# Kernel tuning notes

Hardware: AMD Instinct MI355X
Metric: run time of the kernel (lower is better)

The kernel has to match this reference:

```python
import jax, jax.numpy as jnp
import numpy as np

N = 100_000      # nodes
E = 1_600_000    # edges (avg degree 16)
F_IN = 128       # dataset.num_features
H = 128          # hidden
C = 25_000       # num_clusters (~ target_ratio 0.25 * N)
G = 64           # graphs in batch
NCLS = 10        # dataset.num_classes


def _gcn_conv(x, w, b, src, dst, n):
    # PyG GCNConv: add self loops, symmetric normalization deg^-1/2 A_hat deg^-1/2
    h = x @ w  # [n, out]
    deg = jnp.zeros((n,), x.dtype).at[dst].add(1.0) + 1.0  # +1 self loop
    dis = jax.lax.rsqrt(deg)
    norm = dis[src] * dis[dst]  # [E]
    out = jnp.zeros_like(h).at[dst].add(h[src] * norm[:, None])
    out = out + h * (dis * dis)[:, None]  # self-loop term norm_ii = deg_i^-1
    return out + b


def _mean_pool(x, seg, num_seg):
    s = jax.ops.segment_sum(x, seg, num_segments=num_seg)
    cnt = jax.ops.segment_sum(jnp.ones((x.shape[0],), x.dtype), seg, num_segments=num_seg)
    return s / jnp.maximum(cnt, 1.0)[:, None]


def _max_pool(x, seg, num_seg):
    m = jax.ops.segment_max(x, seg, num_segments=num_seg)
    cnt = jax.ops.segment_sum(jnp.ones((x.shape[0],), x.dtype), seg, num_segments=num_seg)
    return jnp.where(cnt[:, None] > 0, m, 0.0)


def setup_inputs() -> dict:
    key = jax.random.key(0)
    ks = jax.random.split(key, 12)
    def glorot(k, shape):
        fan_in = shape[0]
        return (jax.random.normal(k, shape, jnp.float32) / np.sqrt(fan_in)).astype(jnp.float32)
    return {
        "x": jax.random.normal(ks[0], (N, F_IN), jnp.float32),
        "edge_index": jax.random.randint(ks[1], (2, E), 0, N, dtype=jnp.int32).astype(jnp.int64),
        "batch": jnp.sort(jax.random.randint(ks[2], (N,), 0, G, dtype=jnp.int32)).astype(jnp.int64),
        "cluster": jax.random.randint(ks[3], (N,), 0, C, dtype=jnp.int32).astype(jnp.int64),
        "num_clusters": C,
        "num_graphs": G,
        "W1": glorot(ks[4], (F_IN, H)), "b1": jnp.zeros((H,), jnp.float32),
        "W2": glorot(ks[5], (H, H)),   "b2": jnp.zeros((H,), jnp.float32),
        "W3": glorot(ks[6], (H, H)),   "b3": jnp.zeros((H,), jnp.float32),
        "lin1_w": glorot(ks[7], (4 * H, H)), "lin1_b": jnp.zeros((H,), jnp.float32),
        "lin2_w": glorot(ks[8], (H, NCLS)),  "lin2_b": jnp.zeros((NCLS,), jnp.float32),
    }


def reference(x, edge_index, batch, cluster, num_clusters, num_graphs,
              W1, b1, W2, b2, W3, b3, lin1_w, lin1_b, lin2_w, lin2_b):
    n = x.shape[0]
    src, dst = edge_index[0], edge_index[1]
    # conv1 + relu (dropout is identity in eval mode)
    h = jax.nn.relu(_gcn_conv(x, W1, b1, src, dst, n))
    pre_mean = _mean_pool(h, batch, num_graphs)
    pre_max = _max_pool(h, batch, num_graphs)
    # LaCorePooling(aggregate='mean'): segment-mean nodes by cluster id,
    # relabel edges to cluster ids, derive pooled batch vector.
    hp = _mean_pool(h, cluster, num_clusters)            # [C, H]
    src_p, dst_p = cluster[src], cluster[dst]            # pooled edge list
    batch_p = jax.ops.segment_max(batch, cluster, num_segments=num_clusters)
    batch_p = jnp.maximum(batch_p, 0)                    # empty clusters -> graph 0
    # post-pool GCN layers
    hp = jax.nn.relu(_gcn_conv(hp, W2, b2, src_p, dst_p, num_clusters))
    hp = jax.nn.relu(_gcn_conv(hp, W3, b3, src_p, dst_p, num_clusters))
    post_mean = _mean_pool(hp, batch_p, num_graphs)
    post_max = _max_pool(hp, batch_p, num_graphs)
    z = jnp.concatenate([pre_mean, pre_max, post_mean, post_max], axis=-1)  # [G, 4H]
    z = jax.nn.relu(z @ lin1_w + lin1_b)
    z = z @ lin2_w + lin2_b
    return jax.nn.log_softmax(z, axis=-1)
```

## Files before the change

### kernel.cpp

```cpp
#include <hip/hip_runtime.h>

constexpr int N_NODES = 100000;
constexpr int N_EDGES = 1600000;
constexpr int N_CLUST = 25000;
constexpr int N_GRAPH = 64;
constexpr int NCLSN   = 10;

constexpr int BKT1_SHIFT = 9;
constexpr int NBKT1 = (N_NODES + 511) / 512;
constexpr int EPB = 4096;
constexpr int NEB = (N_EDGES + EPB - 1) / EPB;
constexpr int SORT_CAP = 12288;

constexpr int SCAN_BPB = 1024;
constexpr int NB1 = (N_NODES + SCAN_BPB - 1) / SCAN_BPB;
constexpr int NB2 = (N_CLUST + SCAN_BPB - 1) / SCAN_BPB;
constexpr int NB3 = (N_CLUST + SCAN_BPB - 1) / SCAN_BPB;
constexpr int NBT = NB1 + NB2 + NB3;

__device__ __forceinline__ float bf16lo(unsigned u){ return __uint_as_float(u << 16); }
__device__ __forceinline__ float bf16hi(unsigned u){ return __uint_as_float(u & 0xffff0000u); }
__device__ __forceinline__ unsigned bf16_rne(float f){
  unsigned u = __float_as_uint(f);
  return (u + 0x7fffu + ((u >> 16) & 1u)) >> 16;
}
__device__ __forceinline__ unsigned pack2(float lo, float hi){
  return bf16_rne(lo) | (bf16_rne(hi) << 16);
}

typedef short bf16x8 __attribute__((ext_vector_type(8)));
typedef float f32x4  __attribute__((ext_vector_type(4)));

__launch_bounds__(1024)
__global__ void count_kernel(const int* __restrict__ ei, int* __restrict__ bhist){
  __shared__ int h1c[NBKT1];
  int t = threadIdx.x;
  for (int i = t; i < NBKT1; i += 1024) h1c[i] = 0;
  __syncthreads();
  int e0 = blockIdx.x * EPB;
  #pragma unroll
  for (int i = 0; i < EPB / 1024; ++i){
    int e = e0 + i * 1024 + t;
    if (e < N_EDGES) atomicAdd(&h1c[ei[N_EDGES + e] >> BKT1_SHIFT], 1);
  }
  __syncthreads();
  for (int i = t; i < NBKT1; i += 1024) bhist[blockIdx.x * NBKT1 + i] = h1c[i];
}

__launch_bounds__(512)
__global__ void colscan(const int* __restrict__ bhist, int* __restrict__ boffs,
                        int* __restrict__ gcnt1){
  __shared__ int s[512];
  int i = blockIdx.x;
  int t = threadIdx.x;
  int v = (t < NEB) ? bhist[t * NBKT1 + i] : 0;
  s[t] = v; __syncthreads();
  for (int o = 1; o < 512; o <<= 1){
    int a = (t >= o) ? s[t - o] : 0;
    __syncthreads(); s[t] += a; __syncthreads();
  }
  if (t < NEB) boffs[t * NBKT1 + i] = s[t] - v;
  if (t == 511) gcnt1[i] = s[511];
}

__launch_bounds__(256)
__global__ void bucket_scan(const int* __restrict__ gcnt1, int* __restrict__ gbase1){
  __shared__ int s[256];
  int t = threadIdx.x;
  int v = (t < NBKT1) ? gcnt1[t] : 0;
  s[t] = v; __syncthreads();
  for (int off = 1; off < 256; off <<= 1){
    int a = (t >= off) ? s[t - off] : 0;
    __syncthreads(); s[t] += a; __syncthreads();
  }
  if (t < NBKT1) gbase1[t] = s[t] - v;
}

__launch_bounds__(1024)
__global__ void scatter_kernel(const int* __restrict__ ei, const int* __restrict__ gbase1,
                               const int* __restrict__ boffs, unsigned int* __restrict__ stage1){
  __shared__ int gb1[NBKT1];
  __shared__ int cur[NBKT1];
  int t = threadIdx.x, b = blockIdx.x;
  for (int i = t; i < NBKT1; i += 1024){
    gb1[i] = gbase1[i] + boffs[b * NBKT1 + i];
    cur[i] = 0;
  }
  __syncthreads();
  int e0 = b * EPB;
  #pragma unroll
  for (int i = 0; i < EPB / 1024; ++i){
    int e = e0 + i * 1024 + t;
    if (e < N_EDGES){
      int src = ei[e], dst = ei[N_EDGES + e];
      int bk = dst >> BKT1_SHIFT;
      int r = atomicAdd(&cur[bk], 1);
      stage1[gb1[bk] + r] = ((unsigned)(dst & 511) << 17) | (unsigned)src;
    }
  }
}

__launch_bounds__(1024)
__global__ void bucket_sort(const unsigned int* __restrict__ stage, const int* __restrict__ gbase,
                            const int* __restrict__ gcnt, int* __restrict__ outpay,
                            int* __restrict__ deg){
  __shared__ int cnt[512], off[512];
  __shared__ int sorted[SORT_CAP];
  int b = blockIdx.x, t = threadIdx.x;
  int base = gbase[b], n = gcnt[b];
  if (t < 512) cnt[t] = 0;
  __syncthreads();
  for (int i = t; i < n; i += 1024) atomicAdd(&cnt[stage[base + i] >> 17], 1);
  __syncthreads();
  if (t < 512){
    int idx = b * 512 + t;
    if (idx < N_NODES) deg[idx] = cnt[t];
    off[t] = cnt[t];
  }
  __syncthreads();
  for (int s = 1; s < 512; s <<= 1){
    int v = 0;
    if (t < 512 && t >= s) v = off[t - s];
    __syncthreads();
    if (t < 512) off[t] += v;
    __syncthreads();
  }
  if (t < 512) off[t] -= cnt[t];
  __syncthreads();
  if (n <= SORT_CAP){
    for (int i = t; i < n; i += 1024){
      unsigned w = stage[base + i];
      int r = atomicAdd(&off[w >> 17], 1);
      sorted[r] = (int)(w & 0x1FFFFu);
    }
    __syncthreads();
    for (int i = t; i < n; i += 1024) outpay[base + i] = sorted[i];
  } else {
    for (int i = t; i < n; i += 1024){
      unsigned w = stage[base + i];
      int r = atomicAdd(&off[w >> 17], 1);
      outpay[base + r] = (int)(w & 0x1FFFFu);
    }
  }
}

__global__ void node_prep(const int* __restrict__ cluster, const int* __restrict__ deg1,
                          int* __restrict__ cntn, int* __restrict__ deg2){
  int v = blockIdx.x * blockDim.x + threadIdx.x;
  if (v < N_NODES){
    int c = cluster[v];
    atomicAdd(&cntn[c], 1);
    atomicAdd(&deg2[c], deg1[v]);
  }
}

__device__ __forceinline__ void seg_select(int b, const int* deg1, const int* cntn,
                                           const int* deg2, const int*& src, int& n, int& base){
  if (b < NB1){ src = deg1; n = N_NODES; base = b * SCAN_BPB; }
  else if (b < NB1 + NB2){ src = cntn; n = N_CLUST; base = (b - NB1) * SCAN_BPB; }
  else { src = deg2; n = N_CLUST; base = (b - NB1 - NB2) * SCAN_BPB; }
}

__launch_bounds__(256)
__global__ void block_sums(const int* __restrict__ deg1, const int* __restrict__ cntn,
                           const int* __restrict__ deg2, int* __restrict__ bsum){
  int b = blockIdx.x;
  const int* src; int n, base;
  seg_select(b, deg1, cntn, deg2, src, n, base);
  int t = threadIdx.x;
  int i0 = base + t * 4;
  int s = 0;
  if (i0 + 3 < n){ int4 v = *(const int4*)&src[i0]; s = v.x + v.y + v.z + v.w; }
  else { for (int j = 0; j < 4; ++j){ int i = i0 + j; if (i < n) s += src[i]; } }
  __shared__ int sh[256];
  sh[t] = s; __syncthreads();
  for (int off = 128; off > 0; off >>= 1){
    if (t < off) sh[t] += sh[t + off];
    __syncthreads();
  }
  if (t == 0) bsum[b] = sh[0];
}

__launch_bounds__(256)
__global__ void scan_bsums(const int* __restrict__ bsum, int* __restrict__ boff,
                           int* __restrict__ rowptr1, int* __restrict__ rowptrn,
                           int* __restrict__ rowptr2){
  __shared__ int s[256];
  int t = threadIdx.x;
  int v = (t < NBT) ? bsum[t] : 0;
  s[t] = v; __syncthreads();
  int seg = (t < NB1) ? 0 : (t < NB1 + NB2 ? 1 : 2);
  for (int off = 1; off < 256; off <<= 1){
    int add = 0;
    if (t >= off){
      int u = t - off;
      int useg = (u < NB1) ? 0 : (u < NB1 + NB2 ? 1 : 2);
      if (useg == seg) add = s[u];
    }
    __syncthreads();
    s[t] += add;
    __syncthreads();
  }
  if (t < NBT) boff[t] = s[t] - v;
  if (t == NB1 - 1)       rowptr1[N_NODES] = s[t];
  if (t == NB1 + NB2 - 1) rowptrn[N_CLUST] = s[t];
  if (t == NBT - 1)       rowptr2[N_CLUST] = s[t];
}

__launch_bounds__(256)
__global__ void scan_final(const int* __restrict__ deg1, const int* __restrict__ cntn,
                           const int* __restrict__ deg2, const int* __restrict__ boff,
                           int* __restrict__ rowptr1, float* __restrict__ dis1,
                           int* __restrict__ rowptrn, int* __restrict__ curn,
                           int* __restrict__ rowptr2, float* __restrict__ dis2){
  int b = blockIdx.x;
  const int* src; int n, base;
  seg_select(b, deg1, cntn, deg2, src, n, base);
  int* rp; int* cur; float* dis;
  if (b < NB1){ rp = rowptr1; cur = nullptr; dis = dis1; }
  else if (b < NB1 + NB2){ rp = rowptrn; cur = curn; dis = nullptr; }
  else { rp = rowptr2; cur = nullptr; dis = dis2; }
  int t = threadIdx.x;
  int i0 = base + t * 4;
  int v[4]; int s = 0;
  #pragma unroll
  for (int j = 0; j < 4; ++j){ int i = i0 + j; v[j] = (i < n) ? src[i] : 0; s += v[j]; }
  __shared__ int sh[256];
  sh[t] = s; __syncthreads();
  for (int off = 1; off < 256; off <<= 1){
    int add = (t >= off) ? sh[t - off] : 0;
    __syncthreads();
    sh[t] += add;
    __syncthreads();
  }
  int run = sh[t] - s + boff[b];
  #pragma unroll
  for (int j = 0; j < 4; ++j){
    int i = i0 + j;
    if (i < n){
      rp[i] = run;
      if (cur) cur[i] = run;
      if (dis) dis[i] = rsqrtf((float)v[j] + 1.0f);
      run += v[j];
    }
  }
}

__global__ void fill_n(const int* __restrict__ cluster, int* __restrict__ curn,
                       int* __restrict__ nidx){
  int v = blockIdx.x * blockDim.x + threadIdx.x;
  if (v >= N_NODES) return;
  nidx[atomicAdd(&curn[cluster[v]], 1)] = v;
}

__launch_bounds__(256)
__global__ void psrc_build(const int* __restrict__ rowptrn, const int* __restrict__ nidx,
                           const int* __restrict__ rowptr1, const int* __restrict__ esrc1,
                           const int* __restrict__ cluster, const int* __restrict__ rowptr2,
                           int* __restrict__ psrcC){
  int c = blockIdx.x * 4 + (threadIdx.x >> 6);
  int l = threadIdx.x & 63;
  int mb = rowptrn[c], me = rowptrn[c + 1];
  int cnt = me - mb;
  int base_l = 0, d_l = 0;
  if (l < cnt){
    int v = nidx[mb + l];
    base_l = rowptr1[v];
    d_l = rowptr1[v + 1] - base_l;
  }
  int pref = d_l;
  #pragma unroll
  for (int off = 1; off < 64; off <<= 1){
    int u = __shfl_up(pref, off);
    if (l >= off) pref += u;
  }
  int total = __shfl(pref, 63);
  int wbase = rowptr2[c];
  int iters = (total + 63) >> 6;
  for (int k = 0; k < iters; ++k){
    int idx = k * 64 + l;
    int idxc = min(idx, total - 1);
    int m = 0;
    for (int j = 0; j < cnt; ++j){
      int pj = __shfl(pref, j);
      if (idxc >= pj) m = j + 1;
    }
    int pm = __shfl(pref, m);
    int dm = __shfl(d_l, m);
    int bm = __shfl(base_l, m);
    int e = bm + idxc - (pm - dm);
    int sc = cluster[esrc1[e]];
    if (idx < total) psrcC[wbase + idx] = sc;
  }
}

template<bool A_BF16>
__launch_bounds__(256)
__global__ void gemm_mfma(const void* __restrict__ Aptr, const float* __restrict__ B,
                          const float* __restrict__ scale, unsigned* __restrict__ Cmat,
                          int M){
  __shared__ __align__(16) unsigned Blds[128 * 68];
  __shared__ __align__(16) unsigned Alds[64 * 68];
  const int t = threadIdx.x;
  const int row0 = blockIdx.x * 64;

  #pragma unroll
  for (int i = 0; i < 8; ++i){
    int task = t + i * 256;
    int kp = task >> 5, nq = task & 31;
    float4 b0 = *(const float4*)&B[(2 * kp) * 128 + nq * 4];
    float4 b1 = *(const float4*)&B[(2 * kp + 1) * 128 + nq * 4];
    Blds[(nq * 4 + 0) * 68 + kp] = pack2(b0.x, b1.x);
    Blds[(nq * 4 + 1) * 68 + kp] = pack2(b0.y, b1.y);
    Blds[(nq * 4 + 2) * 68 + kp] = pack2(b0.z, b1.z);
    Blds[(nq * 4 + 3) * 68 + kp] = pack2(b0.w, b1.w);
  }
  if (A_BF16){
    const unsigned* A = (const unsigned*)Aptr;
    #pragma unroll
    for (int i = 0; i < 8; ++i){
      int idx = t + i * 256;
      int row = idx >> 5, c2 = idx & 31;
      int grow = min(row0 + row, M - 1);
      uint2 v = *(const uint2*)&A[(size_t)grow * 64 + c2 * 2];
      Alds[row * 68 + c2 * 2]     = v.x;
      Alds[row * 68 + c2 * 2 + 1] = v.y;
    }
  } else {
    const float* A = (const float*)Aptr;
    #pragma unroll
    for (int i = 0; i < 8; ++i){
      int idx = t + i * 256;
      int row = idx >> 5, k4 = idx & 31;
      int grow = min(row0 + row, M - 1);
      float4 v = *(const float4*)&A[(size_t)grow * 128 + k4 * 4];
      Alds[row * 68 + k4 * 2]     = pack2(v.x, v.y);
      Alds[row * 68 + k4 * 2 + 1] = pack2(v.z, v.w);
    }
  }
  __syncthreads();

  const int wv = t >> 6, l = t & 63, quad = l >> 4, n16 = l & 15;
  f32x4 acc[8];
  #pragma unroll
  for (int nt = 0; nt < 8; ++nt) acc[nt] = (f32x4){0.f, 0.f, 0.f, 0.f};
  const int arow = wv * 16 + n16;
  #pragma unroll
  for (int ks = 0; ks < 4; ++ks){
    bf16x8 af = *(const bf16x8*)&Alds[arow * 68 + ks * 16 + quad * 4];
    #pragma unroll
    for (int nt = 0; nt < 8; ++nt){
      bf16x8 bfr = *(const bf16x8*)&Blds[(nt * 16 + n16) * 68 + ks * 16 + quad * 4];
      acc[nt] = __builtin_amdgcn_mfma_f32_16x16x32_bf16(af, bfr, acc[nt], 0, 0, 0);
    }
  }
  #pragma unroll
  for (int nt = 0; nt < 8; ++nt){
    #pragma unroll
    for (int r = 0; r < 4; ++r){
      int row = row0 + wv * 16 + quad * 4 + r;
      float sc = scale[min(row, M - 1)];
      float v = acc[nt][r] * sc;
      float vhi = __shfl_xor(v, 1);
      if (((l & 1) == 0) && row < M)
        Cmat[(size_t)row * 64 + nt * 8 + (n16 >> 1)] = pack2(v, vhi);
    }
  }
}

__launch_bounds__(256)
__global__ void conv_csr(const unsigned* __restrict__ Ts, const float* __restrict__ dis,
                         const int* __restrict__ rowptr, const int* __restrict__ esrc,
                         const float* __restrict__ bias, unsigned* __restrict__ Hout){
  int w = blockIdx.x * 4 + (threadIdx.x >> 6);
  int l = threadIdx.x & 63;
  int q = l & 15, h = l >> 4;
  int beg = rowptr[w], end = rowptr[w + 1];
  float acc[8] = {0.f,0.f,0.f,0.f,0.f,0.f,0.f,0.f};
  for (int base = beg; base < end; base += 64){
    int n = min(64, end - base);
    int eid = esrc[base + min(l, n - 1)];
    int j = 0;
    for (; j + 8 <= n; j += 8){
      int s0 = __shfl(eid, j + h);
      int s1 = __shfl(eid, j + 4 + h);
      uint4 u0 = *(const uint4*)&Ts[(size_t)s0 * 64 + q * 4];
      uint4 u1 = *(const uint4*)&Ts[(size_t)s1 * 64 + q * 4];
      acc[0] += bf16lo(u0.x); acc[1] += bf16hi(u0.x);
      acc[2] += bf16lo(u0.y); acc[3] += bf16hi(u0.y);
      acc[4] += bf16lo(u0.z); acc[5] += bf16hi(u0.z);
      acc[6] += bf16lo(u0.w); acc[7] += bf16hi(u0.w);
      acc[0] += bf16lo(u1.x); acc[1] += bf16hi(u1.x);
      acc[2] += bf16lo(u1.y); acc[3] += bf16hi(u1.y);
      acc[4] += bf16lo(u1.z); acc[5] += bf16hi(u1.z);
      acc[6] += bf16lo(u1.w); acc[7] += bf16hi(u1.w);
    }
    for (; j < n; j += 4){
      int ei = j + h;
      int s = __shfl(eid, min(ei, n - 1));
      uint4 u = *(const uint4*)&Ts[(size_t)s * 64 + q * 4];
      if (ei < n){
        acc[0] += bf16lo(u.x); acc[1] += bf16hi(u.x);
        acc[2] += bf16lo(u.y); acc[3] += bf16hi(u.y);
        acc[4] += bf16lo(u.z); acc[5] += bf16hi(u.z);
        acc[6] += bf16lo(u.w); acc[7] += bf16hi(u.w);
      }
    }
  }
  #pragma unroll
  for (int k = 0; k < 8; ++k){
    acc[k] += __shfl_xor(acc[k], 16);
    acc[k] += __shfl_xor(acc[k], 32);
  }
  float d = dis[w];
  uint4 us = *(const uint4*)&Ts[(size_t)w * 64 + q * 4];
  float4 b0 = *(const float4*)&bias[q * 8];
  float4 b1 = *(const float4*)&bias[q * 8 + 4];
  float r0 = fmaxf(fmaf(d, acc[0] + bf16lo(us.x), b0.x), 0.f);
  float r1 = fmaxf(fmaf(d, acc[1] + bf16hi(us.x), b0.y), 0.f);
  float r2 = fmaxf(fmaf(d, acc[2] + bf16lo(us.y), b0.z), 0.f);
  float r3 = fmaxf(fmaf(d, acc[3] + bf16hi(us.y), b0.w), 0.f);
  float r4 = fmaxf(fmaf(d, acc[4] + bf16lo(us.z), b1.x), 0.f);
  float r5 = fmaxf(fmaf(d, acc[5] + bf16hi(us.z), b1.y), 0.f);
  float r6 = fmaxf(fmaf(d, acc[6] + bf16lo(us.w), b1.z), 0.f);
  float r7 = fmaxf(fmaf(d, acc[7] + bf16hi(us.w), b1.w), 0.f);
  if (h == 0){
    uint4 o;
    o.x = pack2(r0, r1); o.y = pack2(r2, r3);
    o.z = pack2(r4, r5); o.w = pack2(r6, r7);
    *(uint4*)&Hout[(size_t)w * 64 + q * 4] = o;
  }
}

__launch_bounds__(256)
__global__ void cluster_gather(const unsigned* __restrict__ h1, const int* __restrict__ rowptrn,
                               const int* __restrict__ nidx, const int* __restrict__ batch,
                               unsigned* __restrict__ hp, int* __restrict__ batchp){
  int c = blockIdx.x * 4 + (threadIdx.x >> 6);
  int l = threadIdx.x & 63;
  int q = l & 15, h = l >> 4;
  int mb = rowptrn[c], me = rowptrn[c + 1];
  float acc[8] = {0.f,0.f,0.f,0.f,0.f,0.f,0.f,0.f};
  int vmax = -1;
  for (int base = mb; base < me; base += 64){
    int n = min(64, me - base);
    int vid = nidx[base + min(l, n - 1)];
    if (l < n) vmax = max(vmax, vid);
    int j = 0;
    for (; j + 8 <= n; j += 8){
      int s0 = __shfl(vid, j + h);
      int s1 = __shfl(vid, j + 4 + h);
      uint4 u0 = *(const uint4*)&h1[(size_t)s0 * 64 + q * 4];
      uint4 u1 = *(const uint4*)&h1[(size_t)s1 * 64 + q * 4];
      acc[0] += bf16lo(u0.x); acc[1] += bf16hi(u0.x);
      acc[2] += bf16lo(u0.y); acc[3] += bf16hi(u0.y);
      acc[4] += bf16lo(u0.z); acc[5] += bf16hi(u0.z);
      acc[6] += bf16lo(u0.w); acc[7] += bf16hi(u0.w);
      acc[0] += bf16lo(u1.x); acc[1] += bf16hi(u1.x);
      acc[2] += bf16lo(u1.y); acc[3] += bf16hi(u1.y);
      acc[4] += bf16lo(u1.z); acc[5] += bf16hi(u1.z);
      acc[6] += bf16lo(u1.w); acc[7] += bf16hi(u1.w);
    }
    for (; j < n; j += 4){
      int ei = j + h;
      int s = __shfl(vid, min(ei, n - 1));
      uint4 u = *(const uint4*)&h1[(size_t)s * 64 + q * 4];
      if (ei < n){
        acc[0] += bf16lo(u.x); acc[1] += bf16hi(u.x);
        acc[2] += bf16lo(u.y); acc[3] += bf16hi(u.y);
        acc[4] += bf16lo(u.z); acc[5] += bf16hi(u.z);
        acc[6] += bf16lo(u.w); acc[7] += bf16hi(u.w);
      }
    }
  }
  #pragma unroll
  for (int k = 0; k < 8; ++k){
    acc[k] += __shfl_xor(acc[k], 16);
    acc[k] += __shfl_xor(acc[k], 32);
  }
  #pragma unroll
  for (int off = 32; off > 0; off >>= 1) vmax = max(vmax, __shfl_xor(vmax, off));
  float inv = 1.0f / (float)max(me - mb, 1);
  if (h == 0){
    uint4 o;
    o.x = pack2(acc[0] * inv, acc[1] * inv);
    o.y = pack2(acc[2] * inv, acc[3] * inv);
    o.z = pack2(acc[4] * inv, acc[5] * inv);
    o.w = pack2(acc[6] * inv, acc[7] * inv);
    *(uint4*)&hp[(size_t)c * 64 + q * 4] = o;
  }
  if (l == 0) batchp[c] = (vmax >= 0) ? batch[vmax] : 0;
}

__global__ void cntp_kernel(const int* __restrict__ batchp, int* __restrict__ cntp){
  int c = blockIdx.x * blockDim.x + threadIdx.x;
  if (c < N_CLUST) atomicAdd(&cntp[batchp[c]], 1);
}

__global__ void scan_cntp(const int* __restrict__ cntp, int* __restrict__ gbasep,
                          int* __restrict__ curp){
  int t = threadIdx.x;
  int v = cntp[t];
  int s = v;
  for (int off = 1; off < 64; off <<= 1){
    int u = __shfl_up(s, off);
    if (t >= off) s += u;
  }
  gbasep[t] = s - v; curp[t] = s - v;
  if (t == 63) gbasep[64] = s;
}

__global__ void fill_c(const int* __restrict__ batchp, int* __restrict__ curp,
                       int* __restrict__ cidx){
  int c = blockIdx.x * blockDim.x + threadIdx.x;
  if (c < N_CLUST) cidx[atomicAdd(&curp[batchp[c]], 1)] = c;
}

__global__ void graph_bounds(const int* __restrict__ batch, int* __restrict__ gstart){
  int g = threadIdx.x;
  if (g > N_GRAPH) return;
  int lo = 0, hi = N_NODES;
  while (lo < hi){ int mid = (lo + hi) >> 1; if (batch[mid] < g) lo = mid + 1; else hi = mid; }
  gstart[g] = lo;
}

__device__ __forceinline__ void atomicMaxPosF(float* addr, float v){
  atomicMax((int*)addr, __float_as_int(v));
}

constexpr int PRE_SPLIT = 8;
__launch_bounds__(256)
__global__ void pre_pool_g(const unsigned* __restrict__ h1, const int* __restrict__ gstart,
                           float* __restrict__ psum, float* __restrict__ pmax){
  int g = blockIdx.x / PRE_SPLIT, sp = blockIdx.x % PRE_SPLIT;
  int t = threadIdx.x, w = t >> 6, l = t & 63;
  int s0 = gstart[g], s1 = gstart[g + 1];
  int n = s1 - s0;
  int per = (n + PRE_SPLIT - 1) / PRE_SPLIT;
  int b0 = s0 + sp * per, b1 = min(b0 + per, s1);
  float2 a0{0.f,0.f}, a1{0.f,0.f}, a2{0.f,0.f}, a3{0.f,0.f};
  float2 mx{0.f,0.f};
  int i = b0 + w;
  for (; i + 12 < b1; i += 16){
    unsigned u0 = h1[(size_t)(i     ) * 64 + l];
    unsigned u1 = h1[(size_t)(i +  4) * 64 + l];
    unsigned u2 = h1[(size_t)(i +  8) * 64 + l];
    unsigned u3 = h1[(size_t)(i + 12) * 64 + l];
    float f0x = bf16lo(u0), f0y = bf16hi(u0);
    float f1x = bf16lo(u1), f1y = bf16hi(u1);
    float f2x = bf16lo(u2), f2y = bf16hi(u2);
    float f3x = bf16lo(u3), f3y = bf16hi(u3);
    a0.x += f0x; a0.y += f0y; a1.x += f1x; a1.y += f1y;
    a2.x += f2x; a2.y += f2y; a3.x += f3x; a3.y += f3y;
    mx.x = fmaxf(fmaxf(mx.x, fmaxf(f0x, f1x)), fmaxf(f2x, f3x));
    mx.y = fmaxf(fmaxf(mx.y, fmaxf(f0y, f1y)), fmaxf(f2y, f3y));
  }
  for (; i < b1; i += 4){
    unsigned u = h1[(size_t)i * 64 + l];
    float fx = bf16lo(u), fy = bf16hi(u);
    a0.x += fx; a0.y += fy;
    mx.x = fmaxf(mx.x, fx); mx.y = fmaxf(mx.y, fy);
  }
  __shared__ float2 ssum[4][64], smax[4][64];
  ssum[w][l] = { a0.x + a1.x + a2.x + a3.x, a0.y + a1.y + a2.y + a3.y };
  smax[w][l] = mx;
  __syncthreads();
  if (w == 0){
    float2 S = ssum[0][l], M = smax[0][l];
    #pragma unroll
    for (int k = 1; k < 4; ++k){
      S.x += ssum[k][l].x; S.y += ssum[k][l].y;
      M.x = fmaxf(M.x, smax[k][l].x); M.y = fmaxf(M.y, smax[k][l].y);
    }
    atomicAdd(&psum[g * 128 + 2 * l], S.x);
    atomicAdd(&psum[g * 128 + 2 * l + 1], S.y);
    atomicMaxPosF(&pmax[g * 128 + 2 * l], M.x);
    atomicMaxPosF(&pmax[g * 128 + 2 * l + 1], M.y);
  }
}

constexpr int POST_SPLIT = 4;
__launch_bounds__(256)
__global__ void post_pool_g(const unsigned* __restrict__ hp3, const int* __restrict__ gbasep,
                            const int* __restrict__ cidx,
                            float* __restrict__ psum, float* __restrict__ pmax){
  int g = blockIdx.x / POST_SPLIT, sp = blockIdx.x % POST_SPLIT;
  int t = threadIdx.x, w = t >> 6, l = t & 63;
  int s0 = gbasep[g], s1 = gbasep[g + 1];
  int n = s1 - s0;
  int per = (n + POST_SPLIT * 4 - 1) / (POST_SPLIT * 4);
  int b0 = s0 + (sp * 4 + w) * per, b1 = min(b0 + per, s1);
  float2 a0{0.f,0.f}, a1{0.f,0.f}, a2{0.f,0.f}, a3{0.f,0.f};
  float2 mx{0.f,0.f};
  for (int base = b0; base < b1; base += 64){
    int nn = min(64, b1 - base);
    int cid = cidx[base + min(l, nn - 1)];
    int j = 0;
    for (; j + 4 <= nn; j += 4){
      int c0 = __shfl(cid, j);
      int c1 = __shfl(cid, j + 1);
      int c2 = __shfl(cid, j + 2);
      int c3 = __shfl(cid, j + 3);
      unsigned u0 = hp3[(size_t)c0 * 64 + l];
      unsigned u1 = hp3[(size_t)c1 * 64 + l];
      unsigned u2 = hp3[(size_t)c2 * 64 + l];
      unsigned u3 = hp3[(size_t)c3 * 64 + l];
      float f0x = bf16lo(u0), f0y = bf16hi(u0);
      float f1x = bf16lo(u1), f1y = bf16hi(u1);
      float f2x = bf16lo(u2), f2y = bf16hi(u2);
      float f3x = bf16lo(u3), f3y = bf16hi(u3);
      a0.x += f0x; a0.y += f0y; a1.x += f1x; a1.y += f1y;
      a2.x += f2x; a2.y += f2y; a3.x += f3x; a3.y += f3y;
      mx.x = fmaxf(fmaxf(mx.x, fmaxf(f0x, f1x)), fmaxf(f2x, f3x));
      mx.y = fmaxf(fmaxf(mx.y, fmaxf(f0y, f1y)), fmaxf(f2y, f3y));
    }
    for (; j < nn; ++j){
      int c = __shfl(cid, j);
      unsigned u = hp3[(size_t)c * 64 + l];
      float fx = bf16lo(u), fy = bf16hi(u);
      a0.x += fx; a0.y += fy;
      mx.x = fmaxf(mx.x, fx); mx.y = fmaxf(mx.y, fy);
    }
  }
  __shared__ float2 ssum[4][64], smax[4][64];
  ssum[w][l] = { a0.x + a1.x + a2.x + a3.x, a0.y + a1.y + a2.y + a3.y };
  smax[w][l] = mx;
  __syncthreads();
  if (w == 0){
    float2 S = ssum[0][l], M = smax[0][l];
    #pragma unroll
    for (int k = 1; k < 4; ++k){
      S.x += ssum[k][l].x; S.y += ssum[k][l].y;
      M.x = fmaxf(M.x, smax[k][l].x); M.y = fmaxf(M.y, smax[k][l].y);
    }
    atomicAdd(&psum[g * 128 + 2 * l], S.x);
    atomicAdd(&psum[g * 128 + 2 * l + 1], S.y);
    atomicMaxPosF(&pmax[g * 128 + 2 * l], M.x);
    atomicMaxPosF(&pmax[g * 128 + 2 * l + 1], M.y);
  }
}

__launch_bounds__(128)
__global__ void head_kernel(const float* __restrict__ psum, const float* __restrict__ pmax,
                            const float* __restrict__ postsum, const float* __restrict__ postmax,
                            const int* __restrict__ gstart, const int* __restrict__ cntp,
                            const float* __restrict__ l1w, const float* __restrict__ l1b,
                            const float* __restrict__ l2w, const float* __restrict__ l2b,
                            float* __restrict__ out){
  int g = blockIdx.x, t = threadIdx.x;
  __shared__ float z[512];
  __shared__ float a[128];
  __shared__ float logits[16];
  __shared__ float lse_s;
  float cpre  = (float)max(gstart[g + 1] - gstart[g], 1);
  float cpost = fmaxf((float)cntp[g], 1.0f);
  z[t]       = psum[g * 128 + t] / cpre;
  z[128 + t] = pmax[g * 128 + t];
  z[256 + t] = postsum[g * 128 + t] / cpost;
  z[384 + t] = postmax[g * 128 + t];
  __syncthreads();
  float acc = l1b[t];
  #pragma unroll 8
  for (int k = 0; k < 512; ++k) acc = fmaf(z[k], l1w[k * 128 + t], acc);
  a[t] = fmaxf(acc, 0.f);
  __syncthreads();
  if (t < NCLSN){
    float s2 = l2b[t];
    for (int k = 0; k < 128; ++k) s2 = fmaf(a[k], l2w[k * NCLSN + t], s2);
    logits[t] = s2;
  }
  __syncthreads();
  if (t == 0){
    float m = logits[0];
    for (int c = 1; c < NCLSN; ++c) m = fmaxf(m, logits[c]);
    float s = 0.f;
    for (int c = 0; c < NCLSN; ++c) s += expf(logits[c] - m);
    lse_s = m + logf(s);
  }
  __syncthreads();
  if (t < NCLSN) out[g * NCLSN + t] = logits[t] - lse_s;
}

extern "C" void kernel_launch(void* const* d_in, const int* in_sizes, int n_in,
                              void* d_out, int out_size, void* d_ws, size_t ws_size,
                              hipStream_t stream){
  const float* x       = (const float*)d_in[0];
  const int*   ei      = (const int*)  d_in[1];
  const int*   batch   = (const int*)  d_in[2];
  const int*   cluster = (const int*)  d_in[3];
  const float* W1      = (const float*)d_in[6];
  const float* b1      = (const float*)d_in[7];
  const float* W2      = (const float*)d_in[8];
  const float* b2      = (const float*)d_in[9];
  const float* W3      = (const float*)d_in[10];
  const float* b3      = (const float*)d_in[11];
  const float* l1w     = (const float*)d_in[12];
  const float* l1b     = (const float*)d_in[13];
  const float* l2w     = (const float*)d_in[14];
  const float* l2b     = (const float*)d_in[15];
  float* out = (float*)d_out;

  char* base = (char*)d_ws;
  size_t off = 0;
  auto alloc = [&](size_t bytes) -> char* {
    char* p = base + off;
    off += (bytes + 255) & ~size_t(255);
    return p;
  };
  char*  zbase  = base + off;
  int*   cntn   = (int*)  alloc((size_t)N_CLUST * 4);
  int*   deg2   = (int*)  alloc((size_t)N_CLUST * 4);
  int*   cntp   = (int*)  alloc((size_t)N_GRAPH * 4);
  float* pre_s  = (float*)alloc((size_t)N_GRAPH * 128 * 4);
  float* pre_m  = (float*)alloc((size_t)N_GRAPH * 128 * 4);
  float* post_s = (float*)alloc((size_t)N_GRAPH * 128 * 4);
  float* post_m = (float*)alloc((size_t)N_GRAPH * 128 * 4);
  size_t zsize = off;
  unsigned* Ts1   = (unsigned*)alloc((size_t)N_NODES * 64 * 4);
  unsigned* h1    = (unsigned*)alloc((size_t)N_NODES * 64 * 4);
  int*   esrc1   = (int*)  alloc((size_t)N_EDGES * 4);
  int*   psrcC   = (int*)  alloc((size_t)N_EDGES * 4);
  int*   deg1    = (int*)  alloc((size_t)N_NODES * 4);
  int*   rowptr1 = (int*)  alloc((size_t)(N_NODES + 1) * 4);
  int*   rowptrn = (int*)  alloc((size_t)(N_CLUST + 1) * 4);
  int*   curn    = (int*)  alloc((size_t)N_CLUST * 4);
  int*   rowptr2 = (int*)  alloc((size_t)(N_CLUST + 1) * 4);
  int*   nidx    = (int*)  alloc((size_t)N_NODES * 4);
  float* dis1    = (float*)alloc((size_t)N_NODES * 4);
  float* dis2    = (float*)alloc((size_t)N_CLUST * 4);
  int*   batchp  = (int*)  alloc((size_t)N_CLUST * 4);
  int*   gstart  = (int*)  alloc((size_t)(N_GRAPH + 1) * 4);
  int*   bsum    = (int*)  alloc((size_t)NBT * 4);
  int*   boff    = (int*)  alloc((size_t)NBT * 4);
  int*   gcnt1   = (int*)  alloc((size_t)NBKT1 * 4);
  int*   gbase1  = (int*)  alloc((size_t)NBKT1 * 4);
  int*   bhist   = (int*)  alloc((size_t)NEB * NBKT1 * 4);
  int*   boffs   = (int*)  alloc((size_t)NEB * NBKT1 * 4);
  int*   gbasep  = (int*)  alloc((size_t)(N_GRAPH + 1) * 4);
  int*   curp    = (int*)  alloc((size_t)N_GRAPH * 4);
  int*   cidx    = (int*)  alloc((size_t)N_CLUST * 4);
  unsigned int* stage1 = (unsigned int*)h1;
  unsigned* hp  = Ts1;
  unsigned* Ts2 = Ts1 + (size_t)N_CLUST * 64;
  unsigned* hp2 = Ts1 + (size_t)2 * N_CLUST * 64;
  unsigned* hp3 = Ts1 + (size_t)3 * N_CLUST * 64;
  unsigned* Ts3 = Ts2;

  (void)in_sizes; (void)n_in; (void)out_size; (void)ws_size;

  hipMemsetAsync(zbase, 0, zsize, stream);

  count_kernel  <<<NEB, 1024, 0, stream>>>(ei, bhist);
  colscan       <<<NBKT1, 512, 0, stream>>>(bhist, boffs, gcnt1);
  bucket_scan   <<<1, 256, 0, stream>>>(gcnt1, gbase1);
  scatter_kernel<<<NEB, 1024, 0, stream>>>(ei, gbase1, boffs, stage1);
  bucket_sort   <<<NBKT1, 1024, 0, stream>>>(stage1, gbase1, gcnt1, esrc1, deg1);
  node_prep<<<(N_NODES + 255) / 256, 256, 0, stream>>>(cluster, deg1, cntn, deg2);
  block_sums <<<NBT, 256, 0, stream>>>(deg1, cntn, deg2, bsum);
  scan_bsums <<<1, 256, 0, stream>>>(bsum, boff, rowptr1, rowptrn, rowptr2);
  scan_final <<<NBT, 256, 0, stream>>>(deg1, cntn, deg2, boff,
                                       rowptr1, dis1, rowptrn, curn, rowptr2, dis2);
  fill_n<<<(N_NODES + 255) / 256, 256, 0, stream>>>(cluster, curn, nidx);
  psrc_build<<<N_CLUST / 4, 256, 0, stream>>>(rowptrn, nidx, rowptr1, esrc1,
                                              cluster, rowptr2, psrcC);

  gemm_mfma<false><<<(N_NODES + 63) / 64, 256, 0, stream>>>(x, W1, dis1, Ts1, N_NODES);
  conv_csr<<<N_NODES / 4, 256, 0, stream>>>(Ts1, dis1, rowptr1, esrc1, b1, h1);

  graph_bounds<<<1, 128, 0, stream>>>(batch, gstart);
  pre_pool_g<<<N_GRAPH * PRE_SPLIT, 256, 0, stream>>>(h1, gstart, pre_s, pre_m);

  cluster_gather<<<N_CLUST / 4, 256, 0, stream>>>(h1, rowptrn, nidx, batch, hp, batchp);
  cntp_kernel<<<(N_CLUST + 255) / 256, 256, 0, stream>>>(batchp, cntp);
  scan_cntp<<<1, 64, 0, stream>>>(cntp, gbasep, curp);
  fill_c<<<(N_CLUST + 255) / 256, 256, 0, stream>>>(batchp, curp, cidx);

  gemm_mfma<true><<<(N_CLUST + 63) / 64, 256, 0, stream>>>(hp, W2, dis2, Ts2, N_CLUST);
  conv_csr<<<N_CLUST / 4, 256, 0, stream>>>(Ts2, dis2, rowptr2, psrcC, b2, hp2);

  gemm_mfma<true><<<(N_CLUST + 63) / 64, 256, 0, stream>>>(hp2, W3, dis2, Ts3, N_CLUST);
  conv_csr<<<N_CLUST / 4, 256, 0, stream>>>(Ts3, dis2, rowptr2, psrcC, b3, hp3);

  post_pool_g<<<N_GRAPH * POST_SPLIT, 256, 0, stream>>>(hp3, gbasep, cidx, post_s, post_m);
  head_kernel<<<N_GRAPH, 128, 0, stream>>>(pre_s, pre_m, post_s, post_m, gstart, cntp,
                                           l1w, l1b, l2w, l2b, out);
}
```

Measured before the change: 527.6 us.

## Merge small pipeline kernels into fewer launches via block-range fusion

Cuts the launch chain from about 23 kernels to 13. The memset is folded into extra blocks of the count kernel, and the bucket scan is recomputed redundantly in each scatter and sort block. Node-prep atomics move into bucket_sort, and the block-offset scan moves into scan_final. Independent work (gemm1 with fill_n, conv1 with psrc_build, cluster gather with pre-pool, gemm2 with the cluster CSR build) now shares one grid split by block index. This targets per-launch overhead and serialization gaps, at the cost of redundant scans per block and the single-block cidx fill sitting inside the gemm2 launch.

After: 606.9 us. 15.0% more time.

```diff
diff --git a/kernel.cpp b/kernel.cpp
--- a/kernel.cpp
+++ b/kernel.cpp
@@ -11,6 +11,7 @@
 constexpr int EPB = 4096;
 constexpr int NEB = (N_EDGES + EPB - 1) / EPB;
 constexpr int SORT_CAP = 12288;
+constexpr int NZB = 16;
 
 constexpr int SCAN_BPB = 1024;
 constexpr int NB1 = (N_NODES + SCAN_BPB - 1) / SCAN_BPB;
@@ -18,6 +19,16 @@
 constexpr int NB3 = (N_CLUST + SCAN_BPB - 1) / SCAN_BPB;
 constexpr int NBT = NB1 + NB2 + NB3;
 
+constexpr int G1  = (N_NODES + 63) / 64;
+constexpr int FN  = (N_NODES + 255) / 256;
+constexpr int C1  = N_NODES / 4;
+constexpr int PS  = N_CLUST / 4;
+constexpr int CG  = N_CLUST / 4;
+constexpr int PRE_SPLIT = 8;
+constexpr int PP  = N_GRAPH * PRE_SPLIT;
+constexpr int G2  = (N_CLUST + 63) / 64;
+constexpr int POST_SPLIT = 4;
+
 __device__ __forceinline__ float bf16lo(unsigned u){ return __uint_as_float(u << 16); }
 __device__ __forceinline__ float bf16hi(unsigned u){ return __uint_as_float(u & 0xffff0000u); }
 __device__ __forceinline__ unsigned bf16_rne(float f){
@@ -31,10 +42,23 @@
 typedef short bf16x8 __attribute__((ext_vector_type(8)));
 typedef float f32x4  __attribute__((ext_vector_type(4)));
 
+__device__ __forceinline__ int bsearch_batch(const int* __restrict__ batch, int g){
+  int lo = 0, hi = N_NODES;
+  while (lo < hi){ int mid = (lo + hi) >> 1; if (batch[mid] < g) lo = mid + 1; else hi = mid; }
+  return lo;
+}
+
 __launch_bounds__(1024)
-__global__ void count_kernel(const int* __restrict__ ei, int* __restrict__ bhist){
+__global__ void count_kernel(const int* __restrict__ ei, int* __restrict__ bhist,
+                             uint4* __restrict__ zbase, int zwords4){
+  int t = threadIdx.x;
+  if (blockIdx.x >= NEB){
+    int zb = blockIdx.x - NEB;
+    for (int i = zb * 1024 + t; i < zwords4; i += NZB * 1024)
+      zbase[i] = (uint4){0u, 0u, 0u, 0u};
+    return;
+  }
   __shared__ int h1c[NBKT1];
-  int t = threadIdx.x;
   for (int i = t; i < NBKT1; i += 1024) h1c[i] = 0;
   __syncthreads();
   int e0 = blockIdx.x * EPB;
@@ -63,28 +87,29 @@
   if (t == 511) gcnt1[i] = s[511];
 }
 
-__launch_bounds__(256)
-__global__ void bucket_scan(const int* __restrict__ gcnt1, int* __restrict__ gbase1){
+__device__ __forceinline__ void scan_gcnt(const int* __restrict__ gcnt1, int* s, int t){
+  if (t < 256) s[t] = (t < NBKT1) ? gcnt1[t] : 0;
+  __syncthreads();
+  for (int o = 1; o < 256; o <<= 1){
+    int a = 0;
+    if (t < 256 && t >= o) a = s[t - o];
+    __syncthreads();
+    if (t < 256) s[t] += a;
+    __syncthreads();
+  }
+}
+
+__launch_bounds__(1024)
+__global__ void scatter_kernel(const int* __restrict__ ei, const int* __restrict__ gcnt1,
+                               const int* __restrict__ boffs, unsigned int* __restrict__ stage1){
   __shared__ int s[256];
-  int t = threadIdx.x;
-  int v = (t < NBKT1) ? gcnt1[t] : 0;
-  s[t] = v; __syncthreads();
-  for (int off = 1; off < 256; off <<= 1){
-    int a = (t >= off) ? s[t - off] : 0;
-    __syncthreads(); s[t] += a; __syncthreads();
-  }
-  if (t < NBKT1) gbase1[t] = s[t] - v;
-}
-
-__launch_bounds__(1024)
-__global__ void scatter_kernel(const int* __restrict__ ei, const int* __restrict__ gbase1,
-                               const int* __restrict__ boffs, unsigned int* __restrict__ stage1){
   __shared__ int gb1[NBKT1];
   __shared__ int cur[NBKT1];
   int t = threadIdx.x, b = blockIdx.x;
-  for (int i = t; i < NBKT1; i += 1024){
-    gb1[i] = gbase1[i] + boffs[b * NBKT1 + i];
-    cur[i] = 0;
+  scan_gcnt(gcnt1, s, t);
+  if (t < NBKT1){
+    gb1[t] = (t ? s[t - 1] : 0) + boffs[b * NBKT1 + t];
+    cur[t] = 0;
   }
   __syncthreads();
   int e0 = b * EPB;
@@ -101,15 +126,20 @@
 }
 
 __launch_bounds__(1024)
-__global__ void bucket_sort(const unsigned int* __restrict__ stage, const int* __restrict__ gbase,
-                            const int* __restrict__ gcnt, int* __restrict__ outpay,
-                            int* __restrict__ deg){
+__global__ void bucket_sort(const unsigned int* __restrict__ stage, const int* __restrict__ gcnt1,
+                            int* __restrict__ outpay, int* __restrict__ deg,
+                            const int* __restrict__ cluster, int* __restrict__ cntn,
+                            int* __restrict__ deg2){
+  __shared__ int sg[256];
   __shared__ int cnt[512], off[512];
   __shared__ int sorted[SORT_CAP];
+  __shared__ int baseSh;
   int b = blockIdx.x, t = threadIdx.x;
-  int base = gbase[b], n = gcnt[b];
+  scan_gcnt(gcnt1, sg, t);
+  if (t == 0) baseSh = b ? sg[b - 1] : 0;
   if (t < 512) cnt[t] = 0;
   __syncthreads();
+  int base = baseSh, n = gcnt1[b];
   for (int i = t; i < n; i += 1024) atomicAdd(&cnt[stage[base + i] >> 17], 1);
   __syncthreads();
   if (t < 512){
@@ -118,9 +148,9 @@
     off[t] = cnt[t];
   }
   __syncthreads();
-  for (int s = 1; s < 512; s <<= 1){
+  for (int s2 = 1; s2 < 512; s2 <<= 1){
     int v = 0;
-    if (t < 512 && t >= s) v = off[t - s];
+    if (t < 512 && t >= s2) v = off[t - s2];
     __syncthreads();
     if (t < 512) off[t] += v;
     __syncthreads();
@@ -142,15 +172,13 @@
       outpay[base + r] = (int)(w & 0x1FFFFu);
     }
   }
-}
-
-__global__ void node_prep(const int* __restrict__ cluster, const int* __restrict__ deg1,
-                          int* __restrict__ cntn, int* __restrict__ deg2){
-  int v = blockIdx.x * blockDim.x + threadIdx.x;
-  if (v < N_NODES){
-    int c = cluster[v];
-    atomicAdd(&cntn[c], 1);
-    atomicAdd(&deg2[c], deg1[v]);
+  if (t < 512){
+    int idx = b * 512 + t;
+    if (idx < N_NODES){
+      int c = cluster[idx];
+      atomicAdd(&cntn[c], 1);
+      atomicAdd(&deg2[c], cnt[t]);
+    }
   }
 }
 
@@ -182,45 +210,42 @@
 }
 
 __launch_bounds__(256)
-__global__ void scan_bsums(const int* __restrict__ bsum, int* __restrict__ boff,
-                           int* __restrict__ rowptr1, int* __restrict__ rowptrn,
-                           int* __restrict__ rowptr2){
-  __shared__ int s[256];
+__global__ void scan_final(const int* __restrict__ deg1, const int* __restrict__ cntn,
+                           const int* __restrict__ deg2, const int* __restrict__ bsum,
+                           int* __restrict__ rowptr1, float* __restrict__ dis1,
+                           int* __restrict__ rowptrn, int* __restrict__ curn,
+                           int* __restrict__ rowptr2, float* __restrict__ dis2){
+  int b = blockIdx.x;
   int t = threadIdx.x;
-  int v = (t < NBT) ? bsum[t] : 0;
-  s[t] = v; __syncthreads();
+  __shared__ int sb[256];
+  int bv = (t < NBT) ? bsum[t] : 0;
+  sb[t] = bv; __syncthreads();
   int seg = (t < NB1) ? 0 : (t < NB1 + NB2 ? 1 : 2);
   for (int off = 1; off < 256; off <<= 1){
     int add = 0;
     if (t >= off){
       int u = t - off;
       int useg = (u < NB1) ? 0 : (u < NB1 + NB2 ? 1 : 2);
-      if (useg == seg) add = s[u];
-    }
-    __syncthreads();
-    s[t] += add;
-    __syncthreads();
-  }
-  if (t < NBT) boff[t] = s[t] - v;
-  if (t == NB1 - 1)       rowptr1[N_NODES] = s[t];
-  if (t == NB1 + NB2 - 1) rowptrn[N_CLUST] = s[t];
-  if (t == NBT - 1)       rowptr2[N_CLUST] = s[t];
-}
-
-__launch_bounds__(256)
-__global__ void scan_final(const int* __restrict__ deg1, const int* __restrict__ cntn,
-                           const int* __restrict__ deg2, const int* __restrict__ boff,
-                           int* __restrict__ rowptr1, float* __restrict__ dis1,
-                           int* __restrict__ rowptrn, int* __restrict__ curn,
-                           int* __restrict__ rowptr2, float* __restrict__ dis2){
-  int b = blockIdx.x;
+      if (useg == seg) add = sb[u];
+    }
+    __syncthreads();
+    sb[t] += add;
+    __syncthreads();
+  }
+  if (b == 0){
+    if (t == NB1 - 1)       rowptr1[N_NODES] = sb[t];
+    if (t == NB1 + NB2 - 1) rowptrn[N_CLUST] = sb[t];
+    if (t == NBT - 1)       rowptr2[N_CLUST] = sb[t];
+  }
+  int boff_b = sb[b] - bsum[b];
+  __syncthreads();
+
   const int* src; int n, base;
   seg_select(b, deg1, cntn, deg2, src, n, base);
   int* rp; int* cur; float* dis;
   if (b < NB1){ rp = rowptr1; cur = nullptr; dis = dis1; }
   else if (b < NB1 + NB2){ rp = rowptrn; cur = curn; dis = nullptr; }
   else { rp = rowptr2; cur = nullptr; dis = dis2; }
-  int t = threadIdx.x;
   int i0 = base + t * 4;
   int v[4]; int s = 0;
   #pragma unroll
@@ -233,7 +258,7 @@
     sh[t] += add;
     __syncthreads();
   }
-  int run = sh[t] - s + boff[b];
+  int run = sh[t] - s + boff_b;
   #pragma unroll
   for (int j = 0; j < 4; ++j){
     int i = i0 + j;
@@ -246,63 +271,13 @@
   }
 }
 
-__global__ void fill_n(const int* __restrict__ cluster, int* __restrict__ curn,
-                       int* __restrict__ nidx){
-  int v = blockIdx.x * blockDim.x + threadIdx.x;
-  if (v >= N_NODES) return;
-  nidx[atomicAdd(&curn[cluster[v]], 1)] = v;
-}
-
-__launch_bounds__(256)
-__global__ void psrc_build(const int* __restrict__ rowptrn, const int* __restrict__ nidx,
-                           const int* __restrict__ rowptr1, const int* __restrict__ esrc1,
-                           const int* __restrict__ cluster, const int* __restrict__ rowptr2,
-                           int* __restrict__ psrcC){
-  int c = blockIdx.x * 4 + (threadIdx.x >> 6);
-  int l = threadIdx.x & 63;
-  int mb = rowptrn[c], me = rowptrn[c + 1];
-  int cnt = me - mb;
-  int base_l = 0, d_l = 0;
-  if (l < cnt){
-    int v = nidx[mb + l];
-    base_l = rowptr1[v];
-    d_l = rowptr1[v + 1] - base_l;
-  }
-  int pref = d_l;
-  #pragma unroll
-  for (int off = 1; off < 64; off <<= 1){
-    int u = __shfl_up(pref, off);
-    if (l >= off) pref += u;
-  }
-  int total = __shfl(pref, 63);
-  int wbase = rowptr2[c];
-  int iters = (total + 63) >> 6;
-  for (int k = 0; k < iters; ++k){
-    int idx = k * 64 + l;
-    int idxc = min(idx, total - 1);
-    int m = 0;
-    for (int j = 0; j < cnt; ++j){
-      int pj = __shfl(pref, j);
-      if (idxc >= pj) m = j + 1;
-    }
-    int pm = __shfl(pref, m);
-    int dm = __shfl(d_l, m);
-    int bm = __shfl(base_l, m);
-    int e = bm + idxc - (pm - dm);
-    int sc = cluster[esrc1[e]];
-    if (idx < total) psrcC[wbase + idx] = sc;
-  }
-}
-
 template<bool A_BF16>
-__launch_bounds__(256)
-__global__ void gemm_mfma(const void* __restrict__ Aptr, const float* __restrict__ B,
-                          const float* __restrict__ scale, unsigned* __restrict__ Cmat,
-                          int M){
+__device__ void gemm_body(int bm, const void* __restrict__ Aptr, const float* __restrict__ B,
+                          const float* __restrict__ scale, unsigned* __restrict__ Cmat, int M){
   __shared__ __align__(16) unsigned Blds[128 * 68];
   __shared__ __align__(16) unsigned Alds[64 * 68];
   const int t = threadIdx.x;
-  const int row0 = blockIdx.x * 64;
+  const int row0 = bm * 64;
 
   #pragma unroll
   for (int i = 0; i < 8; ++i){
@@ -368,11 +343,10 @@
   }
 }
 
-__launch_bounds__(256)
-__global__ void conv_csr(const unsigned* __restrict__ Ts, const float* __restrict__ dis,
-                         const int* __restrict__ rowptr, const int* __restrict__ esrc,
-                         const float* __restrict__ bias, unsigned* __restrict__ Hout){
-  int w = blockIdx.x * 4 + (threadIdx.x >> 6);
+__device__ void conv_body(int wblk, const unsigned* __restrict__ Ts, const float* __restrict__ dis,
+                          const int* __restrict__ rowptr, const int* __restrict__ esrc,
+                          const float* __restrict__ bias, unsigned* __restrict__ Hout){
+  int w = wblk * 4 + (threadIdx.x >> 6);
   int l = threadIdx.x & 63;
   int q = l & 15, h = l >> 4;
   int beg = rowptr[w], end = rowptr[w + 1];
@@ -432,154 +406,237 @@
   }
 }
 
+__device__ void psrc_body(int cblk, const int* __restrict__ rowptrn, const int* __restrict__ nidx,
+                          const int* __restrict__ rowptr1, const int* __restrict__ esrc1,
+                          const int* __restrict__ cluster, const int* __restrict__ rowptr2,
+                          int* __restrict__ psrcC){
+  int c = cblk * 4 + (threadIdx.x >> 6);
+  int l = threadIdx.x & 63;
+  int mb = rowptrn[c], me = rowptrn[c + 1];
+  int cnt = me - mb;
+  int base_l = 0, d_l = 0;
+  if (l < cnt){
+    int v = nidx[mb + l];
+    base_l = rowptr1[v];
+    d_l = rowptr1[v + 1] - base_l;
+  }
+  int pref = d_l;
+  #pragma unroll
+  for (int off = 1; off < 64; off <<= 1){
+    int u = __shfl_up(pref, off);
+    if (l >= off) pref += u;
+  }
+  int total = __shfl(pref, 63);
+  int wbase = rowptr2[c];
+  int iters = (total + 63) >> 6;
+  for (int k = 0; k < iters; ++k){
+    int idx = k * 64 + l;
+    int idxc = min(idx, total - 1);
+    int m = 0;
+    for (int j = 0; j < cnt; ++j){
+      int pj = __shfl(pref, j);
+      if (idxc >= pj) m = j + 1;
+    }
+    int pm = __shfl(pref, m);
+    int dm = __shfl(d_l, m);
+    int bm = __shfl(base_l, m);
+    int e = bm + idxc - (pm - dm);
+    int sc = cluster[esrc1[e]];
+    if (idx < total) psrcC[wbase + idx] = sc;
+  }
+}
+
 __launch_bounds__(256)
-__global__ void cluster_gather(const unsigned* __restrict__ h1, const int* __restrict__ rowptrn,
-                               const int* __restrict__ nidx, const int* __restrict__ batch,
-                               unsigned* __restrict__ hp, int* __restrict__ batchp){
-  int c = blockIdx.x * 4 + (threadIdx.x >> 6);
-  int l = threadIdx.x & 63;
-  int q = l & 15, h = l >> 4;
-  int mb = rowptrn[c], me = rowptrn[c + 1];
-  float acc[8] = {0.f,0.f,0.f,0.f,0.f,0.f,0.f,0.f};
-  int vmax = -1;
-  for (int base = mb; base < me; base += 64){
-    int n = min(64, me - base);
-    int vid = nidx[base + min(l, n - 1)];
-    if (l < n) vmax = max(vmax, vid);
-    int j = 0;
-    for (; j + 8 <= n; j += 8){
-      int s0 = __shfl(vid, j + h);
-      int s1 = __shfl(vid, j + 4 + h);
-      uint4 u0 = *(const uint4*)&h1[(size_t)s0 * 64 + q * 4];
-      uint4 u1 = *(const uint4*)&h1[(size_t)s1 * 64 + q * 4];
-      acc[0] += bf16lo(u0.x); acc[1] += bf16hi(u0.x);
-      acc[2] += bf16lo(u0.y); acc[3] += bf16hi(u0.y);
-      acc[4] += bf16lo(u0.z); acc[5] += bf16hi(u0.z);
-      acc[6] += bf16lo(u0.w); acc[7] += bf16hi(u0.w);
-      acc[0] += bf16lo(u1.x); acc[1] += bf16hi(u1.x);
-      acc[2] += bf16lo(u1.y); acc[3] += bf16hi(u1.y);
-      acc[4] += bf16lo(u1.z); acc[5] += bf16hi(u1.z);
-      acc[6] += bf16lo(u1.w); acc[7] += bf16hi(u1.w);
-    }
-    for (; j < n; j += 4){
-      int ei = j + h;
-      int s = __shfl(vid, min(ei, n - 1));
-      uint4 u = *(const uint4*)&h1[(size_t)s * 64 + q * 4];
-      if (ei < n){
-        acc[0] += bf16lo(u.x); acc[1] += bf16hi(u.x);
-        acc[2] += bf16lo(u.y); acc[3] += bf16hi(u.y);
-        acc[4] += bf16lo(u.z); acc[5] += bf16hi(u.z);
-        acc[6] += bf16lo(u.w); acc[7] += bf16hi(u.w);
-      }
-    }
-  }
-  #pragma unroll
-  for (int k = 0; k < 8; ++k){
-    acc[k] += __shfl_xor(acc[k], 16);
-    acc[k] += __shfl_xor(acc[k], 32);
-  }
-  #pragma unroll
-  for (int off = 32; off > 0; off >>= 1) vmax = max(vmax, __shfl_xor(vmax, off));
-  float inv = 1.0f / (float)max(me - mb, 1);
-  if (h == 0){
-    uint4 o;
-    o.x = pack2(acc[0] * inv, acc[1] * inv);
-    o.y = pack2(acc[2] * inv, acc[3] * inv);
-    o.z = pack2(acc[4] * inv, acc[5] * inv);
-    o.w = pack2(acc[6] * inv, acc[7] * inv);
-    *(uint4*)&hp[(size_t)c * 64 + q * 4] = o;
-  }
-  if (l == 0) batchp[c] = (vmax >= 0) ? batch[vmax] : 0;
-}
-
-__global__ void cntp_kernel(const int* __restrict__ batchp, int* __restrict__ cntp){
-  int c = blockIdx.x * blockDim.x + threadIdx.x;
-  if (c < N_CLUST) atomicAdd(&cntp[batchp[c]], 1);
-}
-
-__global__ void scan_cntp(const int* __restrict__ cntp, int* __restrict__ gbasep,
-                          int* __restrict__ curp){
-  int t = threadIdx.x;
-  int v = cntp[t];
-  int s = v;
-  for (int off = 1; off < 64; off <<= 1){
-    int u = __shfl_up(s, off);
-    if (t >= off) s += u;
-  }
-  gbasep[t] = s - v; curp[t] = s - v;
-  if (t == 63) gbasep[64] = s;
-}
-
-__global__ void fill_c(const int* __restrict__ batchp, int* __restrict__ curp,
-                       int* __restrict__ cidx){
-  int c = blockIdx.x * blockDim.x + threadIdx.x;
-  if (c < N_CLUST) cidx[atomicAdd(&curp[batchp[c]], 1)] = c;
-}
-
-__global__ void graph_bounds(const int* __restrict__ batch, int* __restrict__ gstart){
-  int g = threadIdx.x;
-  if (g > N_GRAPH) return;
-  int lo = 0, hi = N_NODES;
-  while (lo < hi){ int mid = (lo + hi) >> 1; if (batch[mid] < g) lo = mid + 1; else hi = mid; }
-  gstart[g] = lo;
+__global__ void gemm1_filln(const float* __restrict__ x, const float* __restrict__ W1,
+                            const float* __restrict__ dis1, unsigned* __restrict__ Ts1,
+                            const int* __restrict__ cluster, int* __restrict__ curn,
+                            int* __restrict__ nidx){
+  if (blockIdx.x < G1){
+    gemm_body<false>(blockIdx.x, x, W1, dis1, Ts1, N_NODES);
+  } else {
+    int v = (blockIdx.x - G1) * 256 + threadIdx.x;
+    if (v < N_NODES) nidx[atomicAdd(&curn[cluster[v]], 1)] = v;
+  }
+}
+
+__launch_bounds__(256)
+__global__ void conv1_psrc(const unsigned* __restrict__ Ts1, const float* __restrict__ dis1,
+                           const int* __restrict__ rowptr1, const int* __restrict__ esrc1,
+                           const float* __restrict__ b1, unsigned* __restrict__ h1,
+                           const int* __restrict__ rowptrn, const int* __restrict__ nidx,
+                           const int* __restrict__ cluster, const int* __restrict__ rowptr2,
+                           int* __restrict__ psrcC){
+  if (blockIdx.x < C1)
+    conv_body(blockIdx.x, Ts1, dis1, rowptr1, esrc1, b1, h1);
+  else
+    psrc_body(blockIdx.x - C1, rowptrn, nidx, rowptr1, esrc1, cluster, rowptr2, psrcC);
 }
 
 __device__ __forceinline__ void atomicMaxPosF(float* addr, float v){
   atomicMax((int*)addr, __float_as_int(v));
 }
 
-constexpr int PRE_SPLIT = 8;
 __launch_bounds__(256)
-__global__ void pre_pool_g(const unsigned* __restrict__ h1, const int* __restrict__ gstart,
-                           float* __restrict__ psum, float* __restrict__ pmax){
-  int g = blockIdx.x / PRE_SPLIT, sp = blockIdx.x % PRE_SPLIT;
-  int t = threadIdx.x, w = t >> 6, l = t & 63;
-  int s0 = gstart[g], s1 = gstart[g + 1];
-  int n = s1 - s0;
-  int per = (n + PRE_SPLIT - 1) / PRE_SPLIT;
-  int b0 = s0 + sp * per, b1 = min(b0 + per, s1);
-  float2 a0{0.f,0.f}, a1{0.f,0.f}, a2{0.f,0.f}, a3{0.f,0.f};
-  float2 mx{0.f,0.f};
-  int i = b0 + w;
-  for (; i + 12 < b1; i += 16){
-    unsigned u0 = h1[(size_t)(i     ) * 64 + l];
-    unsigned u1 = h1[(size_t)(i +  4) * 64 + l];
-    unsigned u2 = h1[(size_t)(i +  8) * 64 + l];
-    unsigned u3 = h1[(size_t)(i + 12) * 64 + l];
-    float f0x = bf16lo(u0), f0y = bf16hi(u0);
-    float f1x = bf16lo(u1), f1y = bf16hi(u1);
-    float f2x = bf16lo(u2), f2y = bf16hi(u2);
-    float f3x = bf16lo(u3), f3y = bf16hi(u3);
-    a0.x += f0x; a0.y += f0y; a1.x += f1x; a1.y += f1y;
-    a2.x += f2x; a2.y += f2y; a3.x += f3x; a3.y += f3y;
-    mx.x = fmaxf(fmaxf(mx.x, fmaxf(f0x, f1x)), fmaxf(f2x, f3x));
-    mx.y = fmaxf(fmaxf(mx.y, fmaxf(f0y, f1y)), fmaxf(f2y, f3y));
-  }
-  for (; i < b1; i += 4){
-    unsigned u = h1[(size_t)i * 64 + l];
-    float fx = bf16lo(u), fy = bf16hi(u);
-    a0.x += fx; a0.y += fy;
-    mx.x = fmaxf(mx.x, fx); mx.y = fmaxf(mx.y, fy);
-  }
-  __shared__ float2 ssum[4][64], smax[4][64];
-  ssum[w][l] = { a0.x + a1.x + a2.x + a3.x, a0.y + a1.y + a2.y + a3.y };
-  smax[w][l] = mx;
-  __syncthreads();
-  if (w == 0){
-    float2 S = ssum[0][l], M = smax[0][l];
+__global__ void cluster_pre(const unsigned* __restrict__ h1, const int* __restrict__ rowptrn,
+                            const int* __restrict__ nidx, const int* __restrict__ batch,
+                            unsigned* __restrict__ hp, int* __restrict__ batchp,
+                            int* __restrict__ cntp,
+                            float* __restrict__ psum, float* __restrict__ pmax){
+  if (blockIdx.x < CG){
+    int c = blockIdx.x * 4 + (threadIdx.x >> 6);
+    int l = threadIdx.x & 63;
+    int q = l & 15, h = l >> 4;
+    int mb = rowptrn[c], me = rowptrn[c + 1];
+    float acc[8] = {0.f,0.f,0.f,0.f,0.f,0.f,0.f,0.f};
+    int vmax = -1;
+    for (int base = mb; base < me; base += 64){
+      int n = min(64, me - base);
+      int vid = nidx[base + min(l, n - 1)];
+      if (l < n) vmax = max(vmax, vid);
+      int j = 0;
+      for (; j + 8 <= n; j += 8){
+        int s0 = __shfl(vid, j + h);
+        int s1 = __shfl(vid, j + 4 + h);
+        uint4 u0 = *(const uint4*)&h1[(size_t)s0 * 64 + q * 4];
+        uint4 u1 = *(const uint4*)&h1[(size_t)s1 * 64 + q * 4];
+        acc[0] += bf16lo(u0.x); acc[1] += bf16hi(u0.x);
+        acc[2] += bf16lo(u0.y); acc[3] += bf16hi(u0.y);
+        acc[4] += bf16lo(u0.z); acc[5] += bf16hi(u0.z);
+        acc[6] += bf16lo(u0.w); acc[7] += bf16hi(u0.w);
+        acc[0] += bf16lo(u1.x); acc[1] += bf16hi(u1.x);
+        acc[2] += bf16lo(u1.y); acc[3] += bf16hi(u1.y);
+        acc[4] += bf16lo(u1.z); acc[5] += bf16hi(u1.z);
+        acc[6] += bf16lo(u1.w); acc[7] += bf16hi(u1.w);
+      }
+      for (; j < n; j += 4){
+        int ei = j + h;
+        int s = __shfl(vid, min(ei, n - 1));
+        uint4 u = *(const uint4*)&h1[(size_t)s * 64 + q * 4];
+        if (ei < n){
+          acc[0] += bf16lo(u.x); acc[1] += bf16hi(u.x);
+          acc[2] += bf16lo(u.y); acc[3] += bf16hi(u.y);
+          acc[4] += bf16lo(u.z); acc[5] += bf16hi(u.z);
+          acc[6] += bf16lo(u.w); acc[7] += bf16hi(u.w);
+        }
+      }
+    }
     #pragma unroll
-    for (int k = 1; k < 4; ++k){
-      S.x += ssum[k][l].x; S.y += ssum[k][l].y;
-      M.x = fmaxf(M.x, smax[k][l].x); M.y = fmaxf(M.y, smax[k][l].y);
-    }
-    atomicAdd(&psum[g * 128 + 2 * l], S.x);
-    atomicAdd(&psum[g * 128 + 2 * l + 1], S.y);
-    atomicMaxPosF(&pmax[g * 128 + 2 * l], M.x);
-    atomicMaxPosF(&pmax[g * 128 + 2 * l + 1], M.y);
-  }
-}
-
-constexpr int POST_SPLIT = 4;
+    for (int k = 0; k < 8; ++k){
+      acc[k] += __shfl_xor(acc[k], 16);
+      acc[k] += __shfl_xor(acc[k], 32);
+    }
+    #pragma unroll
+    for (int off = 32; off > 0; off >>= 1) vmax = max(vmax, __shfl_xor(vmax, off));
+    float inv = 1.0f / (float)max(me - mb, 1);
+    if (h == 0){
+      uint4 o;
+      o.x = pack2(acc[0] * inv, acc[1] * inv);
+      o.y = pack2(acc[2] * inv, acc[3] * inv);
+      o.z = pack2(acc[4] * inv, acc[5] * inv);
+      o.w = pack2(acc[6] * inv, acc[7] * inv);
+      *(uint4*)&hp[(size_t)c * 64 + q * 4] = o;
+    }
+    if (l == 0){
+      int bp = (vmax >= 0) ? batch[vmax] : 0;
+      batchp[c] = bp;
+      atomicAdd(&cntp[bp], 1);
+    }
+  } else {
+    int bid = blockIdx.x - CG;
+    int g = bid / PRE_SPLIT, sp = bid % PRE_SPLIT;
+    int t = threadIdx.x, w = t >> 6, l = t & 63;
+    int s0 = bsearch_batch(batch, g), s1 = bsearch_batch(batch, g + 1);
+    int n = s1 - s0;
+    int per = (n + PRE_SPLIT - 1) / PRE_SPLIT;
+    int b0 = s0 + sp * per, b1 = min(b0 + per, s1);
+    float2 a0{0.f,0.f}, a1{0.f,0.f}, a2{0.f,0.f}, a3{0.f,0.f};
+    float2 mx{0.f,0.f};
+    int i = b0 + w;
+    for (; i + 12 < b1; i += 16){
+      unsigned u0 = h1[(size_t)(i     ) * 64 + l];
+      unsigned u1 = h1[(size_t)(i +  4) * 64 + l];
+      unsigned u2 = h1[(size_t)(i +  8) * 64 + l];
+      unsigned u3 = h1[(size_t)(i + 12) * 64 + l];
+      float f0x = bf16lo(u0), f0y = bf16hi(u0);
+      float f1x = bf16lo(u1), f1y = bf16hi(u1);
+      float f2x = bf16lo(u2), f2y = bf16hi(u2);
+      float f3x = bf16lo(u3), f3y = bf16hi(u3);
+      a0.x += f0x; a0.y += f0y; a1.x += f1x; a1.y += f1y;
+      a2.x += f2x; a2.y += f2y; a3.x += f3x; a3.y += f3y;
+      mx.x = fmaxf(fmaxf(mx.x, fmaxf(f0x, f1x)), fmaxf(f2x, f3x));
+      mx.y = fmaxf(fmaxf(mx.y, fmaxf(f0y, f1y)), fmaxf(f2y, f3y));
+    }
+    for (; i < b1; i += 4){
+      unsigned u = h1[(size_t)i * 64 + l];
+      float fx = bf16lo(u), fy = bf16hi(u);
+      a0.x += fx; a0.y += fy;
+      mx.x = fmaxf(mx.x, fx); mx.y = fmaxf(mx.y, fy);
+    }
+    __shared__ float2 ssum[4][64], smax[4][64];
+    ssum[w][l] = { a0.x + a1.x + a2.x + a3.x, a0.y + a1.y + a2.y + a3.y };
+    smax[w][l] = mx;
+    __syncthreads();
+    if (w == 0){
+      float2 S = ssum[0][l], M = smax[0][l];
+      #pragma unroll
+      for (int k = 1; k < 4; ++k){
+        S.x += ssum[k][l].x; S.y += ssum[k][l].y;
+        M.x = fmaxf(M.x, smax[k][l].x); M.y = fmaxf(M.y, smax[k][l].y);
+      }
+      atomicAdd(&psum[g * 128 + 2 * l], S.x);
+      atomicAdd(&psum[g * 128 + 2 * l + 1], S.y);
+      atomicMaxPosF(&pmax[g * 128 + 2 * l], M.x);
+      atomicMaxPosF(&pmax[g * 128 + 2 * l + 1], M.y);
+    }
+  }
+}
+
+__launch_bounds__(256)
+__global__ void gemm2_ccsr(const unsigned* __restrict__ hp, const float* __restrict__ W2,
+                           const float* __restrict__ dis2, unsigned* __restrict__ Ts2,
+                           const int* __restrict__ cntp, const int* __restrict__ batchp,
+                           int* __restrict__ gbasep, int* __restrict__ cidx){
+  if (blockIdx.x < G2){
+    gemm_body<true>(blockIdx.x, hp, W2, dis2, Ts2, N_CLUST);
+  } else {
+    __shared__ int curL[64];
+    int t = threadIdx.x;
+    if (t < 64){
+      int v = cntp[t];
+      int s = v;
+      #pragma unroll
+      for (int off = 1; off < 64; off <<= 1){
+        int u = __shfl_up(s, off);
+        if (t >= off) s += u;
+      }
+      curL[t] = s - v;
+      gbasep[t] = s - v;
+      if (t == 63) gbasep[64] = s;
+    }
+    __syncthreads();
+    for (int c0 = 0; c0 < N_CLUST; c0 += 256){
+      int c = c0 + t;
+      if (c < N_CLUST){
+        int r = atomicAdd(&curL[batchp[c]], 1);
+        cidx[r] = c;
+      }
+    }
+  }
+}
+
+__launch_bounds__(256)
+__global__ void conv_k(const unsigned* __restrict__ Ts, const float* __restrict__ dis,
+                       const int* __restrict__ rowptr, const int* __restrict__ esrc,
+                       const float* __restrict__ bias, unsigned* __restrict__ Hout){
+  conv_body(blockIdx.x, Ts, dis, rowptr, esrc, bias, Hout);
+}
+
+__launch_bounds__(256)
+__global__ void gemm_k(const unsigned* __restrict__ A, const float* __restrict__ B,
+                       const float* __restrict__ scale, unsigned* __restrict__ Cmat, int M){
+  gemm_body<true>(blockIdx.x, A, B, scale, Cmat, M);
+}
+
 __launch_bounds__(256)
 __global__ void post_pool_g(const unsigned* __restrict__ hp3, const int* __restrict__ gbasep,
                             const int* __restrict__ cidx,
@@ -643,7 +700,7 @@
 __launch_bounds__(128)
 __global__ void head_kernel(const float* __restrict__ psum, const float* __restrict__ pmax,
                             const float* __restrict__ postsum, const float* __restrict__ postmax,
-                            const int* __restrict__ gstart, const int* __restrict__ cntp,
+                            const int* __restrict__ batch, const int* __restrict__ cntp,
                             const float* __restrict__ l1w, const float* __restrict__ l1b,
                             const float* __restrict__ l2w, const float* __restrict__ l2b,
                             float* __restrict__ out){
@@ -652,7 +709,8 @@
   __shared__ float a[128];
   __shared__ float logits[16];
   __shared__ float lse_s;
-  float cpre  = (float)max(gstart[g + 1] - gstart[g], 1);
+  int gs0 = bsearch_batch(batch, g), gs1 = bsearch_batch(batch, g + 1);
+  float cpre  = (float)max(gs1 - gs0, 1);
   float cpost = fmaxf((float)cntp[g], 1.0f);
   z[t]       = psum[g * 128 + t] / cpre;
   z[128 + t] = pmax[g * 128 + t];
@@ -729,15 +787,11 @@
   float* dis1    = (float*)alloc((size_t)N_NODES * 4);
   float* dis2    = (float*)alloc((size_t)N_CLUST * 4);
   int*   batchp  = (int*)  alloc((size_t)N_CLUST * 4);
-  int*   gstart  = (int*)  alloc((size_t)(N_GRAPH + 1) * 4);
   int*   bsum    = (int*)  alloc((size_t)NBT * 4);
-  int*   boff    = (int*)  alloc((size_t)NBT * 4);
   int*   gcnt1   = (int*)  alloc((size_t)NBKT1 * 4);
-  int*   gbase1  = (int*)  alloc((size_t)NBKT1 * 4);
   int*   bhist   = (int*)  alloc((size_t)NEB * NBKT1 * 4);
   int*   boffs   = (int*)  alloc((size_t)NEB * NBKT1 * 4);
   int*   gbasep  = (int*)  alloc((size_t)(N_GRAPH + 1) * 4);
-  int*   curp    = (int*)  alloc((size_t)N_GRAPH * 4);
   int*   cidx    = (int*)  alloc((size_t)N_CLUST * 4);
   unsigned int* stage1 = (unsigned int*)h1;
   unsigned* hp  = Ts1;
@@ -748,40 +802,25 @@
 
   (void)in_sizes; (void)n_in; (void)out_size; (void)ws_size;
 
-  hipMemsetAsync(zbase, 0, zsize, stream);
-
-  count_kernel  <<<NEB, 1024, 0, stream>>>(ei, bhist);
-  colscan       <<<NBKT1, 512, 0, stream>>>(bhist, boffs, gcnt1);
-  bucket_scan   <<<1, 256, 0, stream>>>(gcnt1, gbase1);
-  scatter_kernel<<<NEB, 1024, 0, stream>>>(ei, gbase1, boffs, stage1);
-  bucket_sort   <<<NBKT1, 1024, 0, stream>>>(stage1, gbase1, gcnt1, esrc1, deg1);
-  node_prep<<<(N_NODES + 255) / 256, 256, 0, stream>>>(cluster, deg1, cntn, deg2);
-  block_sums <<<NBT, 256, 0, stream>>>(deg1, cntn, deg2, bsum);
-  scan_bsums <<<1, 256, 0, stream>>>(bsum, boff, rowptr1, rowptrn, rowptr2);
-  scan_final <<<NBT, 256, 0, stream>>>(deg1, cntn, deg2, boff,
-                                       rowptr1, dis1, rowptrn, curn, rowptr2, dis2);
-  fill_n<<<(N_NODES + 255) / 256, 256, 0, stream>>>(cluster, curn, nidx);
-  psrc_build<<<N_CLUST / 4, 256, 0, stream>>>(rowptrn, nidx, rowptr1, esrc1,
-                                              cluster, rowptr2, psrcC);
-
-  gemm_mfma<false><<<(N_NODES + 63) / 64, 256, 0, stream>>>(x, W1, dis1, Ts1, N_NODES);
-  conv_csr<<<N_NODES / 4, 256, 0, stream>>>(Ts1, dis1, rowptr1, esrc1, b1, h1);
-
-  graph_bounds<<<1, 128, 0, stream>>>(batch, gstart);
-  pre_pool_g<<<N_GRAPH * PRE_SPLIT, 256, 0, stream>>>(h1, gstart, pre_s, pre_m);
-
-  cluster_gather<<<N_CLUST / 4, 256, 0, stream>>>(h1, rowptrn, nidx, batch, hp, batchp);
-  cntp_kernel<<<(N_CLUST + 255) / 256, 256, 0, stream>>>(batchp, cntp);
-  scan_cntp<<<1, 64, 0, stream>>>(cntp, gbasep, curp);
-  fill_c<<<(N_CLUST + 255) / 256, 256, 0, stream>>>(batchp, curp, cidx);
-
-  gemm_mfma<true><<<(N_CLUST + 63) / 64, 256, 0, stream>>>(hp, W2, dis2, Ts2, N_CLUST);
-  conv_csr<<<N_CLUST / 4, 256, 0, stream>>>(Ts2, dis2, rowptr2, psrcC, b2, hp2);
-
-  gemm_mfma<true><<<(N_CLUST + 63) / 64, 256, 0, stream>>>(hp2, W3, dis2, Ts3, N_CLUST);
-  conv_csr<<<N_CLUST / 4, 256, 0, stream>>>(Ts3, dis2, rowptr2, psrcC, b3, hp3);
-
+  int zwords4 = (int)(zsize / 16);
+
+  count_kernel<<<NEB + NZB, 1024, 0, stream>>>(ei, bhist, (uint4*)zbase, zwords4);
+  colscan<<<NBKT1, 512, 0, stream>>>(bhist, boffs, gcnt1);
+  scatter_kernel<<<NEB, 1024, 0, stream>>>(ei, gcnt1, boffs, stage1);
+  bucket_sort<<<NBKT1, 1024, 0, stream>>>(stage1, gcnt1, esrc1, deg1, cluster, cntn, deg2);
+  block_sums<<<NBT, 256, 0, stream>>>(deg1, cntn, deg2, bsum);
+  scan_final<<<NBT, 256, 0, stream>>>(deg1, cntn, deg2, bsum,
+                                      rowptr1, dis1, rowptrn, curn, rowptr2, dis2);
+  gemm1_filln<<<G1 + FN, 256, 0, stream>>>(x, W1, dis1, Ts1, cluster, curn, nidx);
+  conv1_psrc<<<C1 + PS, 256, 0, stream>>>(Ts1, dis1, rowptr1, esrc1, b1, h1,
+                                          rowptrn, nidx, cluster, rowptr2, psrcC);
+  cluster_pre<<<CG + PP, 256, 0, stream>>>(h1, rowptrn, nidx, batch, hp, batchp, cntp,
+                                           pre_s, pre_m);
+  gemm2_ccsr<<<G2 + 1, 256, 0, stream>>>(hp, W2, dis2, Ts2, cntp, batchp, gbasep, cidx);
+  conv_k<<<N_CLUST / 4, 256, 0, stream>>>(Ts2, dis2, rowptr2, psrcC, b2, hp2);
+  gemm_k<<<G2, 256, 0, stream>>>(hp2, W3, dis2, Ts3, N_CLUST);
+  conv_k<<<N_CLUST / 4, 256, 0, stream>>>(Ts3, dis2, rowptr2, psrcC, b3, hp3);
   post_pool_g<<<N_GRAPH * POST_SPLIT, 256, 0, stream>>>(hp3, gbasep, cidx, post_s, post_m);
-  head_kernel<<<N_GRAPH, 128, 0, stream>>>(pre_s, pre_m, post_s, post_m, gstart, cntp,
+  head_kernel<<<N_GRAPH, 128, 0, stream>>>(pre_s, pre_m, post_s, post_m, batch, cntp,
                                            l1w, l1b, l2w, l2b, out);
 }
```
